# Kernel tuning notes

Measured on AMD Instinct MI355X. Metric: run time of the kernel, lower is better.

The kernel has to match this reference:

```python
import jax, jax.numpy as jnp
import numpy as np

KH, KW = 5, 5  # kernel_size
B, C, H, W = 4, 3, 1024, 1024


def setup_inputs() -> dict:
    key = jax.random.key(0)
    x = jax.random.normal(key, (B, C, H, W), dtype=jnp.float32)
    return {"input": x}


def _median_blur(x, kh, kw):
    # zero padding identical to _compute_zero_padding: (k-1)//2 per side -> 'same' output
    ph, pw = (kh - 1) // 2, (kw - 1) // 2
    b, c, h, w = x.shape
    xp = jnp.pad(x, ((0, 0), (0, 0), (ph, ph), (pw, pw)))
    # Materialize the kh*kw shifted views (same math as conv2d with binary kernel / im2col)
    patches = jnp.stack(
        [xp[:, :, i:i + h, j:j + w] for i in range(kh) for j in range(kw)],
        axis=2,
    )  # [B, C, kh*kw, H, W]
    # torch.median(dim=2)[0]: for odd kh*kw this is the exact middle order statistic
    sorted_p = jnp.sort(patches, axis=2)
    mid = (kh * kw - 1) // 2
    return sorted_p[:, :, mid, :, :]


def reference(input) -> jnp.ndarray:
    return _median_blur(input, KH, KW)
```

## Files before the change

kernel.cpp:

```cpp
#include <hip/hip_runtime.h>

#define CAS(a, b) { float _t = fminf(a, b); (b) = fmaxf(a, b); (a) = _t; }

#define IMG    1024
#define TW     64
#define TH     8
#define RAW_W  72
#define RAW_H  12

__device__ __forceinline__ void sort5(float& a0, float& a1, float& a2, float& a3, float& a4) {
    CAS(a0, a1); CAS(a3, a4); CAS(a2, a4); CAS(a2, a3);
    CAS(a0, a3); CAS(a0, a2); CAS(a1, a4); CAS(a1, a3); CAS(a1, a2);
}

__device__ __forceinline__ float tail13(float a03, float a04,
                                        float a12, float a13, float a14,
                                        float a21, float a22, float a23,
                                        float a30, float a31, float a32,
                                        float a40, float a41) {
    float p = a03, q = a04, r_ = a12, s = a13, t = a14;
    CAS(p, r_); CAS(q, r_); CAS(r_, s);
    float x = a30, y = a31, z = a32, m = a40, n = a41;
    CAS(z, n); CAS(z, m); CAS(y, z);
    CAS(p, n); CAS(q, m); CAS(r_, z); CAS(s, y); CAS(t, x);
    float M01 = fmaxf(p, q),  m01 = fminf(p, q);
    float M23 = fmaxf(r_, s), m23 = fminf(r_, s);
    float max4 = fmaxf(M01, M23);
    float sec4 = fmaxf(fminf(M01, M23), fmaxf(m01, m23));
    float l2 = fmaxf(max4, t);
    float l1 = fmaxf(fminf(max4, t), sec4);
    float mn01 = fminf(n, m),  Mx01 = fmaxf(n, m);
    float mn23 = fminf(z, y),  Mx23 = fmaxf(z, y);
    float min4  = fminf(mn01, mn23);
    float sec4b = fminf(fmaxf(mn01, mn23), fminf(Mx01, Mx23));
    float u1 = fminf(min4, x);
    float u2 = fminf(fmaxf(min4, x), sec4b);
    float E2 = fmaxf(fmaxf(l1, a21), fminf(u1, a23));
    float O1 = __builtin_amdgcn_fmed3f(l2, u2, a22);
    return fminf(E2, O1);
}

__global__ __launch_bounds__(256, 4)
void median5x5_kernel(const float* __restrict__ in, float* __restrict__ out) {
    __shared__ float tile[RAW_H][RAW_W];
    __shared__ float scol[5][TH][RAW_W];

    const int tx  = threadIdx.x;
    const int ty  = threadIdx.y;
    const int tid = ty * 32 + tx;
    const int x0  = blockIdx.x * TW;
    const int y0  = blockIdx.y * TH;
    const float* plane = in + (size_t)blockIdx.z * (IMG * IMG);

    if (tid < RAW_H * (RAW_W / 4)) {
        int r   = tid / 18;
        int k   = tid - r * 18;
        int gy  = y0 - 2 + r;
        int gx0 = x0 - 4 + 4 * k;
        float4 v = make_float4(0.f, 0.f, 0.f, 0.f);
        if ((unsigned)gy < IMG && (unsigned)gx0 < IMG)
            v = *(const float4*)(plane + (size_t)gy * IMG + gx0);
        *(float4*)&tile[r][4 * k] = v;
    }
    __syncthreads();

#define SORTCOL(c) { \
        float c0 = tile[ty + 0][c], c1 = tile[ty + 1][c], c2 = tile[ty + 2][c], \
              c3 = tile[ty + 3][c], c4 = tile[ty + 4][c]; \
        sort5(c0, c1, c2, c3, c4); \
        scol[0][ty][c] = c0; scol[1][ty][c] = c1; scol[2][ty][c] = c2; \
        scol[3][ty][c] = c3; scol[4][ty][c] = c4; }
    SORTCOL(tx + 2);
    SORTCOL(tx + 34);
    if (tx < 4) SORTCOL(tx + 66);
#undef SORTCOL
    __syncthreads();

    const int cb = 2 * tx + 2;
    float v0, v1, v2, v3, v4, v5, m0, m1, m2, m3, t1, t2;

#define LOADROW(i) { \
        const float* rp = &scol[i][ty][cb]; \
        float2 ua = *(const float2*)rp; \
        float2 ub = *(const float2*)(rp + 2); \
        float2 uc = *(const float2*)(rp + 4); \
        v0 = ua.x; v1 = ua.y; v2 = ub.x; v3 = ub.y; v4 = uc.x; v5 = uc.y; \
        m0 = v1; m1 = v2; m2 = v3; m3 = v4; \
        CAS(m0, m1); CAS(m2, m3); CAS(m0, m2); CAS(m1, m3); CAS(m1, m2); }

    LOADROW(0);
    float A03, A04, B03, B04;
    A04 = fmaxf(m3, v0); A03 = fmaxf(fminf(m3, v0), m2);
    B04 = fmaxf(m3, v5); B03 = fmaxf(fminf(m3, v5), m2);

    LOADROW(1);
    float A12, A13, A14, B12, B13, B14;
    A14 = fmaxf(m3, v0); t1 = fminf(m3, v0); A13 = fmaxf(m2, t1); t2 = fminf(m2, t1); A12 = fmaxf(m1, t2);
    B14 = fmaxf(m3, v5); t1 = fminf(m3, v5); B13 = fmaxf(m2, t1); t2 = fminf(m2, t1); B12 = fmaxf(m1, t2);

    LOADROW(2);
    float A21, A22, A23, B21, B22, B23;
    A21 = fmaxf(m0, fminf(m1, v0));
    A22 = __builtin_amdgcn_fmed3f(m1, m2, v0);
    A23 = fminf(m3, fmaxf(m2, v0));
    B21 = fmaxf(m0, fminf(m1, v5));
    B22 = __builtin_amdgcn_fmed3f(m1, m2, v5);
    B23 = fminf(m3, fmaxf(m2, v5));

    LOADROW(3);
    float A30, A31, A32, B30, B31, B32;
    A30 = fminf(m0, v0); t1 = fmaxf(m0, v0); A31 = fminf(m1, t1); t2 = fmaxf(m1, t1); A32 = fminf(m2, t2);
    B30 = fminf(m0, v5); t1 = fmaxf(m0, v5); B31 = fminf(m1, t1); t2 = fmaxf(m1, t1); B32 = fminf(m2, t2);

    LOADROW(4);
    float A40, A41, B40, B41;
    A40 = fminf(m0, v0); A41 = fminf(fmaxf(m0, v0), m1);
    B40 = fminf(m0, v5); B41 = fminf(fmaxf(m0, v5), m1);
#undef LOADROW

    float medA = tail13(A03, A04, A12, A13, A14, A21, A22, A23, A30, A31, A32, A40, A41);
    float medB = tail13(B03, B04, B12, B13, B14, B21, B22, B23, B30, B31, B32, B40, B41);

    float2 o; o.x = medA; o.y = medB;
    *(float2*)(out + (size_t)blockIdx.z * (IMG * IMG) + (size_t)(y0 + ty) * IMG + x0 + 2 * tx) = o;
}

extern "C" void kernel_launch(void* const* d_in, const int* in_sizes, int n_in,
                              void* d_out, int out_size, void* d_ws, size_t ws_size,
                              hipStream_t stream) {
    const float* in  = (const float*)d_in[0];
    float*       out = (float*)d_out;
    dim3 block(32, TH, 1);
    dim3 grid(IMG / TW, IMG / TH, 12);
    hipLaunchKernelGGL(median5x5_kernel, grid, block, 0, stream, in, out);
}
```

Before: 133.3 us.

## Compute four outputs per thread with shared middle sorts and a new merge tail

Widens the tile to 128 columns so each thread produces four adjacent medians, sharing the sorted four-column middle across pairs of outputs. The 13-candidate tail is replaced by a merge-based order-statistic network that uses med3, and the column sort now handles two columns per thread with float2 LDS accesses. The aim is fewer min/max operations and LDS loads per output. The cost is higher register pressure from the 4x13 candidate array and half as many blocks in the grid.

```diff
diff --git a/kernel.cpp b/kernel.cpp
--- a/kernel.cpp
+++ b/kernel.cpp
@@ -1,11 +1,12 @@
 #include <hip/hip_runtime.h>
 
 #define CAS(a, b) { float _t = fminf(a, b); (b) = fmaxf(a, b); (a) = _t; }
+#define MED3(a,b,c) __builtin_amdgcn_fmed3f((a),(b),(c))
 
 #define IMG    1024
-#define TW     64
+#define TW     128
 #define TH     8
-#define RAW_W  72
+#define RAW_W  136
 #define RAW_H  12
 
 __device__ __forceinline__ void sort5(float& a0, float& a1, float& a2, float& a3, float& a4) {
@@ -13,31 +14,32 @@
     CAS(a0, a3); CAS(a0, a2); CAS(a1, a4); CAS(a1, a3); CAS(a1, a2);
 }
 
-__device__ __forceinline__ float tail13(float a03, float a04,
-                                        float a12, float a13, float a14,
-                                        float a21, float a22, float a23,
-                                        float a30, float a31, float a32,
-                                        float a40, float a41) {
-    float p = a03, q = a04, r_ = a12, s = a13, t = a14;
-    CAS(p, r_); CAS(q, r_); CAS(r_, s);
-    float x = a30, y = a31, z = a32, m = a40, n = a41;
-    CAS(z, n); CAS(z, m); CAS(y, z);
-    CAS(p, n); CAS(q, m); CAS(r_, z); CAS(s, y); CAS(t, x);
-    float M01 = fmaxf(p, q),  m01 = fminf(p, q);
-    float M23 = fmaxf(r_, s), m23 = fminf(r_, s);
-    float max4 = fmaxf(M01, M23);
-    float sec4 = fmaxf(fminf(M01, M23), fmaxf(m01, m23));
-    float l2 = fmaxf(max4, t);
-    float l1 = fmaxf(fminf(max4, t), sec4);
-    float mn01 = fminf(n, m),  Mx01 = fmaxf(n, m);
-    float mn23 = fminf(z, y),  Mx23 = fmaxf(z, y);
-    float min4  = fminf(mn01, mn23);
-    float sec4b = fminf(fmaxf(mn01, mn23), fminf(Mx01, Mx23));
-    float u1 = fminf(min4, x);
-    float u2 = fminf(fmaxf(min4, x), sec4b);
-    float E2 = fmaxf(fmaxf(l1, a21), fminf(u1, a23));
-    float O1 = __builtin_amdgcn_fmed3f(l2, u2, a22);
-    return fminf(E2, O1);
+__device__ __forceinline__ float tail13v(const float* cd) {
+    float e0 = cd[0],  e1 = cd[1];
+    float f0 = cd[2],  f1 = cd[3],  f2 = cd[4];
+    float h0 = cd[5],  h1 = cd[6],  h2 = cd[7];
+    float g0 = cd[8],  g1 = cd[9],  g2 = cd[10];
+    float k0 = cd[11], k1 = cd[12];
+
+    float A0 = fminf(e0, f0), M = fmaxf(e0, f0);
+    float A4 = f2;
+    float A3 = fmaxf(e1, f1);
+    float A1 = fminf(fminf(M, e1), f1);
+    float A2 = MED3(e1, f1, M);
+    float C0 = g0;
+    float C4 = fmaxf(g2, k1);
+    float C1 = fminf(g1, k0);
+    float mgk = fminf(g2, k1);
+    float C3 = fmaxf(fmaxf(mgk, g1), k0);
+    float C2 = MED3(g1, k0, mgk);
+    float r3 = fmaxf(fmaxf(fmaxf(fminf(A0, C3), fminf(A1, C2)), fminf(A2, C1)), fminf(A3, C0));
+    float r4 = fmaxf(fmaxf(fmaxf(fminf(A0, C4), fminf(A1, C3)), fminf(A2, C2)),
+                     fmaxf(fminf(A3, C1), fminf(A4, C0)));
+    float r5 = fmaxf(fmaxf(fmaxf(fminf(A1, C4), fminf(A2, C3)), fminf(A3, C2)),
+                     fmaxf(fmaxf(fminf(A4, C1), A0), C0));
+    float r6 = fmaxf(fmaxf(fmaxf(fminf(A2, C4), fminf(A3, C3)), fminf(A4, C2)),
+                     fmaxf(A1, C1));
+    return fmaxf(fmaxf(fmaxf(fminf(r4, h2), fminf(r5, h1)), fminf(r6, h0)), r3);
 }
 
 __global__ __launch_bounds__(256, 4)
@@ -52,9 +54,10 @@
     const int y0  = blockIdx.y * TH;
     const float* plane = in + (size_t)blockIdx.z * (IMG * IMG);
 
-    if (tid < RAW_H * (RAW_W / 4)) {
-        int r   = tid / 18;
-        int k   = tid - r * 18;
+    #pragma unroll
+    for (int t = tid; t < RAW_H * (RAW_W / 4); t += 256) {
+        int r   = t / 34;
+        int k   = t - r * 34;
         int gy  = y0 - 2 + r;
         int gx0 = x0 - 4 + 4 * k;
         float4 v = make_float4(0.f, 0.f, 0.f, 0.f);
@@ -64,65 +67,65 @@
     }
     __syncthreads();
 
-#define SORTCOL(c) { \
-        float c0 = tile[ty + 0][c], c1 = tile[ty + 1][c], c2 = tile[ty + 2][c], \
-              c3 = tile[ty + 3][c], c4 = tile[ty + 4][c]; \
-        sort5(c0, c1, c2, c3, c4); \
-        scol[0][ty][c] = c0; scol[1][ty][c] = c1; scol[2][ty][c] = c2; \
-        scol[3][ty][c] = c3; scol[4][ty][c] = c4; }
-    SORTCOL(tx + 2);
-    SORTCOL(tx + 34);
-    if (tx < 4) SORTCOL(tx + 66);
-#undef SORTCOL
+    for (int p = tx; p < 66; p += 32) {
+        int c = 2 * p + 2;
+        float2 r0 = *(const float2*)&tile[ty + 0][c];
+        float2 r1 = *(const float2*)&tile[ty + 1][c];
+        float2 r2 = *(const float2*)&tile[ty + 2][c];
+        float2 r3 = *(const float2*)&tile[ty + 3][c];
+        float2 r4 = *(const float2*)&tile[ty + 4][c];
+        sort5(r0.x, r1.x, r2.x, r3.x, r4.x);
+        sort5(r0.y, r1.y, r2.y, r3.y, r4.y);
+        *(float2*)&scol[0][ty][c] = r0;
+        *(float2*)&scol[1][ty][c] = r1;
+        *(float2*)&scol[2][ty][c] = r2;
+        *(float2*)&scol[3][ty][c] = r3;
+        *(float2*)&scol[4][ty][c] = r4;
+    }
     __syncthreads();
 
-    const int cb = 2 * tx + 2;
-    float v0, v1, v2, v3, v4, v5, m0, m1, m2, m3, t1, t2;
+    const int cb = 4 * tx + 2;
+    float cd[4][13];
 
-#define LOADROW(i) { \
-        const float* rp = &scol[i][ty][cb]; \
-        float2 ua = *(const float2*)rp; \
-        float2 ub = *(const float2*)(rp + 2); \
-        float2 uc = *(const float2*)(rp + 4); \
-        v0 = ua.x; v1 = ua.y; v2 = ub.x; v3 = ub.y; v4 = uc.x; v5 = uc.y; \
-        m0 = v1; m1 = v2; m2 = v3; m3 = v4; \
-        CAS(m0, m1); CAS(m2, m3); CAS(m0, m2); CAS(m1, m3); CAS(m1, m2); }
+    #pragma unroll
+    for (int i = 0; i < 5; ++i) {
+        const float* rp = &scol[i][ty][cb];
+        float2 u0 = *(const float2*)(rp);
+        float2 u1 = *(const float2*)(rp + 2);
+        float2 u2 = *(const float2*)(rp + 4);
+        float2 u3 = *(const float2*)(rp + 6);
+        float c0 = u0.x, c1 = u0.y, c2 = u1.x, c3 = u1.y;
+        float c4 = u2.x, c5 = u2.y, c6 = u3.x, c7 = u3.y;
 
-    LOADROW(0);
-    float A03, A04, B03, B04;
-    A04 = fmaxf(m3, v0); A03 = fmaxf(fminf(m3, v0), m2);
-    B04 = fmaxf(m3, v5); B03 = fmaxf(fminf(m3, v5), m2);
+        float m0 = c3, m1 = c4; CAS(m0, m1);
+        float a = c1, b = c2; CAS(a, b);
+        float s0 = fminf(a, m0), t1 = fmaxf(a, m0);
+        float t2 = fminf(b, m1), s3 = fmaxf(b, m1);
+        float s1 = fminf(t1, t2), s2 = fmaxf(t1, t2);
+        float d = c5, e = c6; CAS(d, e);
+        float q0 = fminf(m0, d), w1 = fmaxf(m0, d);
+        float w2 = fminf(m1, e), q3 = fmaxf(m1, e);
+        float q1 = fminf(w1, w2), q2 = fmaxf(w1, w2);
 
-    LOADROW(1);
-    float A12, A13, A14, B12, B13, B14;
-    A14 = fmaxf(m3, v0); t1 = fminf(m3, v0); A13 = fmaxf(m2, t1); t2 = fminf(m2, t1); A12 = fmaxf(m1, t2);
-    B14 = fmaxf(m3, v5); t1 = fminf(m3, v5); B13 = fmaxf(m2, t1); t2 = fminf(m2, t1); B12 = fmaxf(m1, t2);
+#define EXT(px, S0, S1, S2, S3, X) { \
+        if (i == 0)      { cd[px][0]  = MED3(S2, S3, X); cd[px][1]  = fmaxf(S3, X); } \
+        else if (i == 1) { cd[px][2]  = MED3(S1, S2, X); cd[px][3]  = MED3(S2, S3, X); cd[px][4] = fmaxf(S3, X); } \
+        else if (i == 2) { cd[px][5]  = MED3(S0, S1, X); cd[px][6]  = MED3(S1, S2, X); cd[px][7] = MED3(S2, S3, X); } \
+        else if (i == 3) { cd[px][8]  = fminf(S0, X);    cd[px][9]  = MED3(S0, S1, X); cd[px][10] = MED3(S1, S2, X); } \
+        else             { cd[px][11] = fminf(S0, X);    cd[px][12] = MED3(S0, S1, X); } }
+        EXT(0, s0, s1, s2, s3, c0)
+        EXT(1, s0, s1, s2, s3, c5)
+        EXT(2, q0, q1, q2, q3, c2)
+        EXT(3, q0, q1, q2, q3, c7)
+#undef EXT
+    }
 
-    LOADROW(2);
-    float A21, A22, A23, B21, B22, B23;
-    A21 = fmaxf(m0, fminf(m1, v0));
-    A22 = __builtin_amdgcn_fmed3f(m1, m2, v0);
-    A23 = fminf(m3, fmaxf(m2, v0));
-    B21 = fmaxf(m0, fminf(m1, v5));
-    B22 = __builtin_amdgcn_fmed3f(m1, m2, v5);
-    B23 = fminf(m3, fmaxf(m2, v5));
-
-    LOADROW(3);
-    float A30, A31, A32, B30, B31, B32;
-    A30 = fminf(m0, v0); t1 = fmaxf(m0, v0); A31 = fminf(m1, t1); t2 = fmaxf(m1, t1); A32 = fminf(m2, t2);
-    B30 = fminf(m0, v5); t1 = fmaxf(m0, v5); B31 = fminf(m1, t1); t2 = fmaxf(m1, t1); B32 = fminf(m2, t2);
-
-    LOADROW(4);
-    float A40, A41, B40, B41;
-    A40 = fminf(m0, v0); A41 = fminf(fmaxf(m0, v0), m1);
-    B40 = fminf(m0, v5); B41 = fminf(fmaxf(m0, v5), m1);
-#undef LOADROW
-
-    float medA = tail13(A03, A04, A12, A13, A14, A21, A22, A23, A30, A31, A32, A40, A41);
-    float medB = tail13(B03, B04, B12, B13, B14, B21, B22, B23, B30, B31, B32, B40, B41);
-
-    float2 o; o.x = medA; o.y = medB;
-    *(float2*)(out + (size_t)blockIdx.z * (IMG * IMG) + (size_t)(y0 + ty) * IMG + x0 + 2 * tx) = o;
+    float4 o;
+    o.x = tail13v(cd[0]);
+    o.y = tail13v(cd[1]);
+    o.z = tail13v(cd[2]);
+    o.w = tail13v(cd[3]);
+    *(float4*)(out + (size_t)blockIdx.z * (IMG * IMG) + (size_t)(y0 + ty) * IMG + x0 + 4 * tx) = o;
 }
 
 extern "C" void kernel_launch(void* const* d_in, const int* in_sizes, int n_in,
```

Result: no change. 135.1 us (+1.4%).
